# Kernel tuning notes

Measured on AMD Instinct MI355X. Metric: run time of the kernel, lower is better.

## Reference

```python
import jax, jax.numpy as jnp
import numpy as np
from jax import lax

B, T, C = 4, 1024, 1024
H, HEAD = 16, 64            # n_head, head size (K == V == HEAD)
TM_DIM, TD_DIM = 32, 64     # TIME_MIX_EXTRA_DIM, W_MIX_EXTRA_DIM
N_LAYER, LAYER_ID = 24, 12
EPS = 1e-5
HEAD_DIV = 8.0              # head_size_divisor


def setup_inputs() -> dict:
    key = jax.random.key(0)
    ks = jax.random.split(key, 10)
    r1 = 1.0 - LAYER_ID / N_LAYER          # ratio_1_to_almost0
    r0 = LAYER_ID / max(N_LAYER - 1, 1)    # ratio_0_to_1
    ddd = np.arange(C, dtype=np.float64) / C
    x_maa = (1.0 - ddd ** r1).astype(np.float32)
    r_maa = (1.0 - ddd ** (0.5 * r1)).astype(np.float32)
    v_maa = (1.0 - (ddd ** r1 + 0.3 * r0)).astype(np.float32)
    n = np.arange(H * HEAD, dtype=np.float64)
    denom = max(H * HEAD - 1, 1)
    time_decay = (-6.0 + 5.0 * (n / denom) ** (0.7 + 1.3 * r0)).reshape(H, HEAD).astype(np.float32)
    zig = (((np.arange(H * HEAD) + 1) % 3) - 1) * 0.1
    time_first = (r0 * (1.0 - n / denom) + zig).reshape(H, HEAD).astype(np.float32)

    def unif(k, shape, s=0.01):
        return jax.random.uniform(k, shape, jnp.float32, -s, s)

    return {
        "x": jax.random.normal(ks[0], (B, T, C), jnp.float32),
        "x_maa": jnp.asarray(x_maa),
        "w_maa": jnp.asarray(x_maa),
        "k_maa": jnp.asarray(x_maa),
        "v_maa": jnp.asarray(v_maa),
        "r_maa": jnp.asarray(r_maa),
        "g_maa": jnp.asarray(r_maa),
        "tm_w1": unif(ks[1], (C, 5 * TM_DIM)),
        "tm_w2": unif(ks[2], (5, TM_DIM, C)),
        "td_w1": unif(ks[3], (C, TD_DIM)),
        "td_w2": unif(ks[4], (TD_DIM, C)),
        "time_decay": jnp.asarray(time_decay),
        "time_first": jnp.asarray(time_first),
        "Wr": jax.random.normal(ks[5], (C, H * HEAD), jnp.float32) * 0.02,
        "Wk": jax.random.normal(ks[6], (C, H * HEAD), jnp.float32) * 0.02,
        "Wv": jax.random.normal(ks[7], (C, H * HEAD), jnp.float32) * 0.02,
        "Wg": jax.random.normal(ks[8], (C, H * HEAD), jnp.float32) * 0.02,
        "Wo": jax.random.normal(ks[9], (H * HEAD, C), jnp.float32) * 0.02,
        "ln_w": jnp.ones((H * HEAD,), jnp.float32),
        "ln_b": jnp.zeros((H * HEAD,), jnp.float32),
    }


def reference(x, x_maa, w_maa, k_maa, v_maa, r_maa, g_maa,
              tm_w1, tm_w2, td_w1, td_w2, time_decay, time_first,
              Wr, Wk, Wv, Wg, Wo, ln_w, ln_b):
    B, T, C = x.shape
    H, K = time_decay.shape
    V = Wv.shape[1] // H
    # token shift: sx = x_{t-1} - x_t (zero-padded at t=0)
    sx = jnp.concatenate([jnp.zeros_like(x[:, :1]), x[:, :-1]], axis=1) - x
    # data-dependent token-mix LoRA: 5 mixing deltas
    mix = jnp.tanh((x + sx * x_maa) @ tm_w1).reshape(B, T, 5, TM_DIM)
    mix = jnp.einsum('btfd,fdc->fbtc', mix, tm_w2)  # [5,B,T,C]
    mw, mk, mv, mr, mg = mix
    wx = x + sx * (w_maa + mw)
    kx = x + sx * (k_maa + mk)
    vx = x + sx * (v_maa + mv)
    rx = x + sx * (r_maa + mr)
    gx = x + sx * (g_maa + mg)
    r = (rx @ Wr).reshape(B, T, H, K)
    k = (kx @ Wk).reshape(B, T, H, K)
    v = (vx @ Wv).reshape(B, T, H, V)
    g = jax.nn.silu(gx @ Wg)                         # [B,T,H*V]
    # data-dependent decay via LoRA, then double-exp squash into (0,1)
    w = time_decay[None, None] + (jnp.tanh(wx @ td_w1) @ td_w2).reshape(B, T, H, K)
    w = jnp.exp(-jnp.exp(w))                         # [B,T,H,K]
    u = time_first                                   # [H,K]

    def step(s, inp):
        rt, kt, vt, wt = inp                         # [B,H,K],[B,H,K],[B,H,V],[B,H,K]
        kv = kt[..., None] * vt[..., None, :]        # [B,H,K,V] outer product
        y = jnp.einsum('bhk,bhkv->bhv', rt, s + u[None, :, :, None] * kv)
        return wt[..., None] * s + kv, y

    s0 = jnp.zeros((B, H, K, V), x.dtype)
    xs = (jnp.moveaxis(r, 1, 0), jnp.moveaxis(k, 1, 0),
          jnp.moveaxis(v, 1, 0), jnp.moveaxis(w, 1, 0))
    _, ys = lax.scan(step, s0, xs)                   # ys: [T,B,H,V]
    out = jnp.moveaxis(ys, 0, 1).reshape(B, T, H, V) / HEAD_DIV
    # GroupNorm with n_kv_head groups over dim_v channels -> per-head norm
    mu = out.mean(-1, keepdims=True)
    var = out.var(-1, keepdims=True)
    out = ((out - mu) * lax.rsqrt(var + EPS)).reshape(B, T, H * V) * ln_w + ln_b
    return (out * g) @ Wo
```

## Files before the change

### kernel.cpp

```cpp
#include <hip/hip_runtime.h>
#include <hip/hip_bf16.h>
#include <math.h>
#include <stdint.h>

constexpr int Bn = 4, Tn = 1024, Cn = 1024, Hn = 16;
constexpr int BT = Bn * Tn;
constexpr long long BTC = (long long)BT * Cn;
constexpr int CL = 64;
constexpr int NC = Tn / CL;

typedef __bf16 bf16x8_t __attribute__((ext_vector_type(8)));
typedef float f32x4_t __attribute__((ext_vector_type(4)));
typedef unsigned short us8_t __attribute__((ext_vector_type(8)));

__device__ __forceinline__ unsigned short f2bf_bits(float v) {
    __hip_bfloat16 h = __float2bfloat16(v);
    return *reinterpret_cast<unsigned short*>(&h);
}
__device__ __forceinline__ float bfbits2f(unsigned short u) {
    unsigned int x = (unsigned int)u << 16;
    return __uint_as_float(x);
}

__device__ __forceinline__ void gload16(const void* g, void* l) {
    auto const* gp = reinterpret_cast<const unsigned int __attribute__((address_space(1)))*>(
        reinterpret_cast<uintptr_t>(g));
    auto* lp = reinterpret_cast<unsigned int __attribute__((address_space(3)))*>(
        reinterpret_cast<uintptr_t>(l));
    __builtin_amdgcn_global_load_lds(gp, lp, 16, 0, 0);
}

__global__ __launch_bounds__(256) void prep_mixin(const float* __restrict__ x,
                                                  const float* __restrict__ x_maa,
                                                  __hip_bfloat16* __restrict__ out) {
    long long q = (long long)blockIdx.x * 256 + threadIdx.x;
    if (q * 4 >= BTC) return;
    long long idx = q * 4;
    int c = (int)(idx & (Cn - 1));
    long long bt = idx >> 10;
    int t = (int)(bt & (Tn - 1));
    float4 xv = *reinterpret_cast<const float4*>(x + idx);
    float4 xp = (t > 0) ? *reinterpret_cast<const float4*>(x + idx - Cn)
                        : make_float4(0.f, 0.f, 0.f, 0.f);
    float4 ma = *reinterpret_cast<const float4*>(x_maa + c);
    ushort4 o;
    o.x = f2bf_bits(xv.x + (xp.x - xv.x) * ma.x);
    o.y = f2bf_bits(xv.y + (xp.y - xv.y) * ma.y);
    o.z = f2bf_bits(xv.z + (xp.z - xv.z) * ma.z);
    o.w = f2bf_bits(xv.w + (xp.w - xv.w) * ma.w);
    *reinterpret_cast<ushort4*>(out + idx) = o;
}

__global__ __launch_bounds__(256) void transp5(const float* __restrict__ W0,
                                               const float* __restrict__ W1,
                                               const float* __restrict__ W2,
                                               const float* __restrict__ W3,
                                               const float* __restrict__ W4,
                                               __hip_bfloat16* __restrict__ T0,
                                               __hip_bfloat16* __restrict__ T1,
                                               __hip_bfloat16* __restrict__ T2,
                                               __hip_bfloat16* __restrict__ T3,
                                               __hip_bfloat16* __restrict__ T4) {
    int z = blockIdx.z;
    const float* W = (z == 0) ? W0 : (z == 1) ? W1 : (z == 2) ? W2 : (z == 3) ? W3 : W4;
    __hip_bfloat16* Wt = (z == 0) ? T0 : (z == 1) ? T1 : (z == 2) ? T2 : (z == 3) ? T3 : T4;
    __shared__ float tile[32][33];
    int c0 = blockIdx.x * 32, r0 = blockIdx.y * 32;
    int tx = threadIdx.x & 31, ty = threadIdx.x >> 5;
    #pragma unroll
    for (int i = 0; i < 4; i++)
        tile[ty + 8 * i][tx] = W[(size_t)(r0 + ty + 8 * i) * Cn + c0 + tx];
    __syncthreads();
    #pragma unroll
    for (int i = 0; i < 4; i++)
        Wt[(size_t)(c0 + ty + 8 * i) * Cn + r0 + tx] = __float2bfloat16(tile[tx][ty + 8 * i]);
}

__global__ __launch_bounds__(256) void transp_bf16(const float* __restrict__ W,
                                                   __hip_bfloat16* __restrict__ Wt,
                                                   int R, int Cc) {
    __shared__ float tile[32][33];
    int c0 = blockIdx.x * 32, r0 = blockIdx.y * 32;
    int tx = threadIdx.x & 31, ty = threadIdx.x >> 5;
    #pragma unroll
    for (int i = 0; i < 4; i++)
        tile[ty + 8 * i][tx] = W[(size_t)(r0 + ty + 8 * i) * Cc + c0 + tx];
    __syncthreads();
    #pragma unroll
    for (int i = 0; i < 4; i++)
        Wt[(size_t)(c0 + ty + 8 * i) * R + r0 + tx] = __float2bfloat16(tile[tx][ty + 8 * i]);
}

template <int EPI>
__global__ __launch_bounds__(256) void gemm_f32(const float* __restrict__ A,
                                                const float* __restrict__ Bm,
                                                float* __restrict__ C,
                                                int M, int N, int K,
                                                const float* __restrict__ extra) {
    __shared__ float As[16][64];
    __shared__ float Bs[16][64];
    int tid = threadIdx.x;
    int m0 = blockIdx.y * 64, n0 = blockIdx.x * 64;
    int tx = tid & 15, ty = tid >> 4;
    int ar = tid >> 2, ac = (tid & 3) * 4;
    int br = tid >> 4, bc = (tid & 15) * 4;
    float acc[4][4] = {};

    for (int k0 = 0; k0 < K; k0 += 16) {
        const float* ap = A + (size_t)(m0 + ar) * K + k0 + ac;
        float4 av = *reinterpret_cast<const float4*>(ap);
        As[ac + 0][ar] = av.x; As[ac + 1][ar] = av.y;
        As[ac + 2][ar] = av.z; As[ac + 3][ar] = av.w;
        float4 bv = *reinterpret_cast<const float4*>(Bm + (size_t)(k0 + br) * N + n0 + bc);
        *reinterpret_cast<float4*>(&Bs[br][bc]) = bv;
        __syncthreads();
        #pragma unroll
        for (int kk = 0; kk < 16; kk++) {
            float4 a4 = *reinterpret_cast<const float4*>(&As[kk][ty * 4]);
            float4 b4 = *reinterpret_cast<const float4*>(&Bs[kk][tx * 4]);
            float aa[4] = {a4.x, a4.y, a4.z, a4.w};
            float bb[4] = {b4.x, b4.y, b4.z, b4.w};
            #pragma unroll
            for (int i = 0; i < 4; i++)
                #pragma unroll
                for (int j = 0; j < 4; j++)
                    acc[i][j] = fmaf(aa[i], bb[j], acc[i][j]);
        }
        __syncthreads();
    }

    #pragma unroll
    for (int i = 0; i < 4; i++) {
        int row = m0 + ty * 4 + i;
        #pragma unroll
        for (int j = 0; j < 4; j++) {
            int col = n0 + tx * 4 + j;
            float v = acc[i][j];
            if (EPI == 3) v = -expf(extra[col] + v);
            C[(size_t)row * N + col] = v;
        }
    }
}

template <int KS>
__global__ __launch_bounds__(256) void gemm_f32_splitk(const float* __restrict__ A,
                                                       const float* __restrict__ Bm,
                                                       float* __restrict__ part,
                                                       int M, int N, int K) {
    __shared__ float As[16][64];
    __shared__ float Bs[16][64];
    int tid = threadIdx.x;
    int kp = blockIdx.x;
    int m0 = blockIdx.y * 64;
    int kbeg = kp * (K / KS), kend = kbeg + K / KS;
    int tx = tid & 15, ty = tid >> 4;
    int ar = tid >> 2, ac = (tid & 3) * 4;
    int br = tid >> 4, bc = (tid & 15) * 4;
    float acc[4][4] = {};

    for (int k0 = kbeg; k0 < kend; k0 += 16) {
        float4 av = *reinterpret_cast<const float4*>(A + (size_t)(m0 + ar) * K + k0 + ac);
        As[ac + 0][ar] = av.x; As[ac + 1][ar] = av.y;
        As[ac + 2][ar] = av.z; As[ac + 3][ar] = av.w;
        *reinterpret_cast<float4*>(&Bs[br][bc]) =
            *reinterpret_cast<const float4*>(Bm + (size_t)(k0 + br) * N + bc);
        __syncthreads();
        #pragma unroll
        for (int kk = 0; kk < 16; kk++) {
            float4 a4 = *reinterpret_cast<const float4*>(&As[kk][ty * 4]);
            float4 b4 = *reinterpret_cast<const float4*>(&Bs[kk][tx * 4]);
            float aa[4] = {a4.x, a4.y, a4.z, a4.w};
            float bb[4] = {b4.x, b4.y, b4.z, b4.w};
            #pragma unroll
            for (int i = 0; i < 4; i++)
                #pragma unroll
                for (int j = 0; j < 4; j++)
                    acc[i][j] = fmaf(aa[i], bb[j], acc[i][j]);
        }
        __syncthreads();
    }
    #pragma unroll
    for (int i = 0; i < 4; i++) {
        int row = m0 + ty * 4 + i;
        #pragma unroll
        for (int j = 0; j < 4; j++)
            part[((size_t)kp * M + row) * N + tx * 4 + j] = acc[i][j];
    }
}

template <int KS>
__global__ __launch_bounds__(256) void splitk_reduce_tanh(const float* __restrict__ part,
                                                          float* __restrict__ outp,
                                                          int total, size_t stride) {
    int i = blockIdx.x * 256 + threadIdx.x;
    if (i >= total) return;
    float s = 0.f;
    #pragma unroll
    for (int kp = 0; kp < KS; kp++) s += part[kp * stride + i];
    outp[i] = tanhf(s);
}

template <int KS>
__global__ __launch_bounds__(256) void splitk_reduce_tanh_bf(const float* __restrict__ part,
                                                             __hip_bfloat16* __restrict__ outp,
                                                             int total, size_t stride) {
    int i = blockIdx.x * 256 + threadIdx.x;
    if (i >= total) return;
    float s = 0.f;
    #pragma unroll
    for (int kp = 0; kp < KS; kp++) s += part[kp * stride + i];
    outp[i] = __float2bfloat16(tanhf(s));
}

template <int KS>
__global__ __launch_bounds__(256) void gemm_mfma_sk(const __hip_bfloat16* __restrict__ A,
                                                    const __hip_bfloat16* __restrict__ Bt,
                                                    float* __restrict__ part,
                                                    int M, int N, int K) {
    __shared__ alignas(16) unsigned short As[64 * 64];
    __shared__ alignas(16) unsigned short Bs[128 * 64];
    int tid = threadIdx.x;
    int m0 = blockIdx.y * 64, n0 = blockIdx.x * 128;
    int kp = blockIdx.z;
    int kbeg = kp * (K / KS), kend = kbeg + K / KS;
    int wave = tid >> 6, lane = tid & 63;
    int wm = (wave & 1) * 32, wn = (wave >> 1) * 64;
    int l15 = lane & 15, l4 = lane >> 4;
    f32x4_t acc[2][4] = {};

    for (int k0 = kbeg; k0 < kend; k0 += 64) {
        #pragma unroll
        for (int p = 0; p < 2; p++) {
            int cch = tid + p * 256;
            int row = cch >> 3, slot = cch & 7;
            int s2 = slot ^ (row & 7);
            *reinterpret_cast<us8_t*>(&As[row * 64 + s2 * 8]) =
                *reinterpret_cast<const us8_t*>(&A[(size_t)(m0 + row) * K + k0 + slot * 8]);
        }
        #pragma unroll
        for (int p = 0; p < 4; p++) {
            int cch = tid + p * 256;
            int row = cch >> 3, slot = cch & 7;
            int s2 = slot ^ (row & 7);
            int rowg = n0 + row; if (rowg > N - 1) rowg = N - 1;
            *reinterpret_cast<us8_t*>(&Bs[row * 64 + s2 * 8]) =
                *reinterpret_cast<const us8_t*>(&Bt[(size_t)rowg * K + k0 + slot * 8]);
        }
        __syncthreads();
        #pragma unroll
        for (int kw = 0; kw < 2; kw++) {
            int slot = kw * 4 + l4;
            bf16x8_t af[2], bfr[4];
            #pragma unroll
            for (int f = 0; f < 2; f++) {
                int ar = wm + f * 16 + l15;
                af[f] = *reinterpret_cast<const bf16x8_t*>(&As[ar * 64 + (slot ^ (ar & 7)) * 8]);
            }
            #pragma unroll
            for (int f = 0; f < 4; f++) {
                int br = wn + f * 16 + l15;
                bfr[f] = *reinterpret_cast<const bf16x8_t*>(&Bs[br * 64 + (slot ^ (br & 7)) * 8]);
            }
            #pragma unroll
            for (int i = 0; i < 2; i++)
                #pragma unroll
                for (int j = 0; j < 4; j++)
                    acc[i][j] = __builtin_amdgcn_mfma_f32_16x16x32_bf16(af[i], bfr[j], acc[i][j], 0, 0, 0);
        }
        __syncthreads();
    }

    #pragma unroll
    for (int i = 0; i < 2; i++) {
        int rbase = m0 + wm + i * 16 + l4 * 4;
        #pragma unroll
        for (int j = 0; j < 4; j++) {
            int col = n0 + wn + j * 16 + l15;
            if (col < N) {
                #pragma unroll
                for (int q = 0; q < 4; q++)
                    part[((size_t)kp * M + rbase + q) * N + col] = acc[i][j][q];
            }
        }
    }
}

__global__ __launch_bounds__(256) void dmix_gemm(const __hip_bfloat16* __restrict__ A,
                                                 const __hip_bfloat16* __restrict__ W2T,
                                                 __hip_bfloat16* __restrict__ D) {
    __shared__ alignas(16) unsigned short As[64 * 32];
    __shared__ alignas(16) unsigned short Bs[128 * 32];
    int tid = threadIdx.x;
    int m0 = blockIdx.x * 64, n0 = blockIdx.y * 128;
    int f  = blockIdx.z;
    int wave = tid >> 6, lane = tid & 63;
    int wm = (wave & 1) * 32, wn = (wave >> 1) * 64;
    int l15 = lane & 15, l4 = lane >> 4;
    int lrow2 = lane >> 2, ls = lane & 3;
    f32x4_t acc[2][4] = {};

    {
        int row = wave * 16 + lrow2;
        int gs = ls ^ (row & 3);
        gload16(&A[(size_t)(m0 + row) * 160 + f * 32 + gs * 8], &As[(wave * 16) * 32]);
    }
    #pragma unroll
    for (int ci = 0; ci < 2; ci++) {
        int r0 = wave * 32 + ci * 16;
        int row = r0 + lrow2;
        int gs = ls ^ (row & 3);
        gload16(&W2T[(size_t)(n0 + row) * 160 + f * 32 + gs * 8], &Bs[r0 * 32]);
    }
    __syncthreads();
    bf16x8_t af[2], bfr[4];
    #pragma unroll
    for (int i = 0; i < 2; i++) {
        int ar = wm + i * 16 + l15;
        af[i] = *reinterpret_cast<const bf16x8_t*>(&As[ar * 32 + ((l4 ^ (ar & 3)) * 8)]);
    }
    #pragma unroll
    for (int j = 0; j < 4; j++) {
        int br = wn + j * 16 + l15;
        bfr[j] = *reinterpret_cast<const bf16x8_t*>(&Bs[br * 32 + ((l4 ^ (br & 3)) * 8)]);
    }
    #pragma unroll
    for (int i = 0; i < 2; i++)
        #pragma unroll
        for (int j = 0; j < 4; j++)
            acc[i][j] = __builtin_amdgcn_mfma_f32_16x16x32_bf16(af[i], bfr[j], acc[i][j], 0, 0, 0);

    __hip_bfloat16* Df = D + (size_t)f * BTC;
    #pragma unroll
    for (int i = 0; i < 2; i++) {
        int rbase = m0 + wm + i * 16 + l4 * 4;
        #pragma unroll
        for (int j = 0; j < 4; j++) {
            int col = n0 + wn + j * 16 + l15;
            #pragma unroll
            for (int q = 0; q < 4; q++)
                Df[(size_t)(rbase + q) * Cn + col] = __float2bfloat16(acc[i][j][q]);
        }
    }
}

__global__ __launch_bounds__(256) void dmix_fuse(const float* __restrict__ x,
                                                 const __hip_bfloat16* __restrict__ D,
                                                 const float* __restrict__ wmaa,
                                                 const float* __restrict__ kmaa,
                                                 const float* __restrict__ vmaa,
                                                 const float* __restrict__ rmaa,
                                                 const float* __restrict__ gmaa,
                                                 float* __restrict__ wx,
                                                 __hip_bfloat16* __restrict__ kxb,
                                                 __hip_bfloat16* __restrict__ vxb,
                                                 __hip_bfloat16* __restrict__ rxb,
                                                 __hip_bfloat16* __restrict__ gxb) {
    long long q = (long long)blockIdx.x * 256 + threadIdx.x;
    if (q * 4 >= BTC) return;
    long long idx = q * 4;
    int c = (int)(idx & (Cn - 1));
    int t = (int)((idx >> 10) & (Tn - 1));
    float4 xv = *reinterpret_cast<const float4*>(x + idx);
    float4 xp = (t > 0) ? *reinterpret_cast<const float4*>(x + idx - Cn)
                        : make_float4(0.f, 0.f, 0.f, 0.f);
    float sx[4] = {xp.x - xv.x, xp.y - xv.y, xp.z - xv.z, xp.w - xv.w};
    float xvv[4] = {xv.x, xv.y, xv.z, xv.w};
    #pragma unroll
    for (int f = 0; f < 5; f++) {
        const float* maa = (f == 0) ? wmaa : (f == 1) ? kmaa : (f == 2) ? vmaa
                         : (f == 3) ? rmaa : gmaa;
        float4 m4 = *reinterpret_cast<const float4*>(maa + c);
        float mm[4] = {m4.x, m4.y, m4.z, m4.w};
        ushort4 d4 = *reinterpret_cast<const ushort4*>(D + (size_t)f * BTC + idx);
        float dd[4] = {bfbits2f(d4.x), bfbits2f(d4.y), bfbits2f(d4.z), bfbits2f(d4.w)};
        float val[4];
        #pragma unroll
        for (int j = 0; j < 4; j++) val[j] = xvv[j] + sx[j] * (mm[j] + dd[j]);
        if (f == 0) {
            *reinterpret_cast<float4*>(wx + idx) = make_float4(val[0], val[1], val[2], val[3]);
        } else {
            ushort4 o;
            o.x = f2bf_bits(val[0]); o.y = f2bf_bits(val[1]);
            o.z = f2bf_bits(val[2]); o.w = f2bf_bits(val[3]);
            __hip_bfloat16* dst = (f == 1) ? kxb : (f == 2) ? vxb : (f == 3) ? rxb : gxb;
            *reinterpret_cast<ushort4*>(dst + idx) = o;
        }
    }
}

__global__ __launch_bounds__(256) void gemm_qkvg(const __hip_bfloat16* __restrict__ A0,
                                                 const __hip_bfloat16* __restrict__ A1,
                                                 const __hip_bfloat16* __restrict__ A2,
                                                 const __hip_bfloat16* __restrict__ A3,
                                                 const __hip_bfloat16* __restrict__ B0,
                                                 const __hip_bfloat16* __restrict__ B1,
                                                 const __hip_bfloat16* __restrict__ B2,
                                                 const __hip_bfloat16* __restrict__ B3,
                                                 __hip_bfloat16* __restrict__ C0,
                                                 __hip_bfloat16* __restrict__ C1,
                                                 __hip_bfloat16* __restrict__ C2,
                                                 __hip_bfloat16* __restrict__ C3,
                                                 int M, int N, int K) {
    int g = blockIdx.z;
    const __hip_bfloat16* A  = (g == 0) ? A0 : (g == 1) ? A1 : (g == 2) ? A2 : A3;
    const __hip_bfloat16* Bt = (g == 0) ? B0 : (g == 1) ? B1 : (g == 2) ? B2 : B3;
    __hip_bfloat16* Co = (g == 0) ? C0 : (g == 1) ? C1 : (g == 2) ? C2 : C3;
    __shared__ alignas(16) unsigned short As[64 * 64];
    __shared__ alignas(16) unsigned short Bs[128 * 64];
    int tid = threadIdx.x;
    int m0 = blockIdx.x * 64, n0 = blockIdx.y * 128;
    int wave = tid >> 6, lane = tid & 63;
    int wm = (wave & 1) * 32, wn = (wave >> 1) * 64;
    int l15 = lane & 15, l4 = lane >> 4;
    int lrow = lane >> 3, ls2 = lane & 7;
    f32x4_t acc[2][4] = {};

    for (int k0 = 0; k0 < K; k0 += 64) {
        #pragma unroll
        for (int ci = 0; ci < 2; ci++) {
            int r0 = wave * 16 + ci * 8;
            int row = r0 + lrow;
            int gs = ls2 ^ (row & 7);
            gload16(&A[(size_t)(m0 + row) * K + k0 + gs * 8], &As[r0 * 64]);
        }
        #pragma unroll
        for (int ci = 0; ci < 4; ci++) {
            int r0 = wave * 32 + ci * 8;
            int row = r0 + lrow;
            int gs = ls2 ^ (row & 7);
            gload16(&Bt[(size_t)(n0 + row) * K + k0 + gs * 8], &Bs[r0 * 64]);
        }
        __syncthreads();
        #pragma unroll
        for (int kw = 0; kw < 2; kw++) {
            int slot = kw * 4 + l4;
            bf16x8_t af[2], bfr[4];
            #pragma unroll
            for (int f = 0; f < 2; f++) {
                int ar = wm + f * 16 + l15;
                af[f] = *reinterpret_cast<const bf16x8_t*>(&As[ar * 64 + (slot ^ (ar & 7)) * 8]);
            }
            #pragma unroll
            for (int f = 0; f < 4; f++) {
                int br = wn + f * 16 + l15;
                bfr[f] = *reinterpret_cast<const bf16x8_t*>(&Bs[br * 64 + (slot ^ (br & 7)) * 8]);
            }
            #pragma unroll
            for (int i = 0; i < 2; i++)
                #pragma unroll
                for (int j = 0; j < 4; j++)
                    acc[i][j] = __builtin_amdgcn_mfma_f32_16x16x32_bf16(af[i], bfr[j], acc[i][j], 0, 0, 0);
        }
        __syncthreads();
    }

    #pragma unroll
    for (int i = 0; i < 2; i++) {
        int rbase = m0 + wm + i * 16 + l4 * 4;
        #pragma unroll
        for (int j = 0; j < 4; j++) {
            int col = n0 + wn + j * 16 + l15;
            #pragma unroll
            for (int q = 0; q < 4; q++) {
                float v = acc[i][j][q];
                if (g == 3) v = v / (1.f + expf(-v));
                Co[(size_t)(rbase + q) * N + col] = __float2bfloat16(v);
            }
        }
    }
}

__global__ __launch_bounds__(256) void gemm_mfma_gl(const __hip_bfloat16* __restrict__ A,
                                                    const __hip_bfloat16* __restrict__ Bt,
                                                    float* __restrict__ Cout,
                                                    int M, int N, int K) {
    __shared__ alignas(16) unsigned short As[64 * 64];
    __shared__ alignas(16) unsigned short Bs[128 * 64];
    int tid = threadIdx.x;
    int m0 = blockIdx.x * 64, n0 = blockIdx.y * 128;
    int wave = tid >> 6, lane = tid & 63;
    int wm = (wave & 1) * 32, wn = (wave >> 1) * 64;
    int l15 = lane & 15, l4 = lane >> 4;
    int lrow = lane >> 3, ls2 = lane & 7;
    f32x4_t acc[2][4] = {};

    for (int k0 = 0; k0 < K; k0 += 64) {
        #pragma unroll
        for (int ci = 0; ci < 2; ci++) {
            int r0 = wave * 16 + ci * 8;
            int row = r0 + lrow;
            int gs = ls2 ^ (row & 7);
            gload16(&A[(size_t)(m0 + row) * K + k0 + gs * 8], &As[r0 * 64]);
        }
        #pragma unroll
        for (int ci = 0; ci < 4; ci++) {
            int r0 = wave * 32 + ci * 8;
            int row = r0 + lrow;
            int gs = ls2 ^ (row & 7);
            gload16(&Bt[(size_t)(n0 + row) * K + k0 + gs * 8], &Bs[r0 * 64]);
        }
        __syncthreads();
        #pragma unroll
        for (int kw = 0; kw < 2; kw++) {
            int slot = kw * 4 + l4;
            bf16x8_t af[2], bfr[4];
            #pragma unroll
            for (int f = 0; f < 2; f++) {
                int ar = wm + f * 16 + l15;
                af[f] = *reinterpret_cast<const bf16x8_t*>(&As[ar * 64 + (slot ^ (ar & 7)) * 8]);
            }
            #pragma unroll
            for (int f = 0; f < 4; f++) {
                int br = wn + f * 16 + l15;
                bfr[f] = *reinterpret_cast<const bf16x8_t*>(&Bs[br * 64 + (slot ^ (br & 7)) * 8]);
            }
            #pragma unroll
            for (int i = 0; i < 2; i++)
                #pragma unroll
                for (int j = 0; j < 4; j++)
                    acc[i][j] = __builtin_amdgcn_mfma_f32_16x16x32_bf16(af[i], bfr[j], acc[i][j], 0, 0, 0);
        }
        __syncthreads();
    }

    #pragma unroll
    for (int i = 0; i < 2; i++) {
        int rbase = m0 + wm + i * 16 + l4 * 4;
        #pragma unroll
        for (int j = 0; j < 4; j++) {
            int col = n0 + wn + j * 16 + l15;
            #pragma unroll
            for (int q = 0; q < 4; q++)
                Cout[(size_t)(rbase + q) * N + col] = acc[i][j][q];
        }
    }
}

__global__ __launch_bounds__(256) void chunk_summary(const __hip_bfloat16* __restrict__ kb,
                                                     const __hip_bfloat16* __restrict__ vb,
                                                     const float* __restrict__ lw,
                                                     float* __restrict__ Bc,
                                                     float* __restrict__ Wtot) {
    int bid = blockIdx.x;
    int c = bid & 15, h = (bid >> 4) & 15, b = bid >> 8;
    size_t gbase = ((size_t)(b * Tn + c * CL) * Hn + h) * 64;
    int tid = threadIdx.x;
    __shared__ float linc[64][68];
    __shared__ float wtp[4][64];
    __shared__ alignas(16) __hip_bfloat16 kdT[64][72];
    __shared__ alignas(16) __hip_bfloat16 vsT[64][72];
    int wave = tid >> 6, lane = tid & 63;
    {
        float acc = 0.f;
        #pragma unroll
        for (int i = 0; i < 16; i++) {
            int t = wave * 16 + i;
            acc += lw[gbase + (size_t)t * 1024 + lane];
            linc[t][lane] = acc;
        }
        wtp[wave][lane] = acc;
    }
    __syncthreads();
    {
        float off = 0.f;
        for (int g = 0; g < wave; g++) off += wtp[g][lane];
        #pragma unroll
        for (int i = 0; i < 16; i++) linc[wave * 16 + i][lane] += off;
    }
    __syncthreads();
    int t4 = tid >> 2, c0 = (tid & 3) * 16;
    #pragma unroll
    for (int i = 0; i < 4; i++) {
        int ch = c0 + i * 4;
        size_t ga = gbase + (size_t)t4 * 1024 + ch;
        ushort4 ku = *reinterpret_cast<const ushort4*>(kb + ga);
        ushort4 vu = *reinterpret_cast<const ushort4*>(vb + ga);
        float kk[4] = {bfbits2f(ku.x), bfbits2f(ku.y), bfbits2f(ku.z), bfbits2f(ku.w)};
        float vv[4] = {bfbits2f(vu.x), bfbits2f(vu.y), bfbits2f(vu.z), bfbits2f(vu.w)};
        #pragma unroll
        for (int j = 0; j < 4; j++) {
            float li = linc[t4][ch + j];
            float lend = linc[63][ch + j];
            kdT[ch + j][t4] = __float2bfloat16(kk[j] * expf(lend - li));
            vsT[ch + j][t4] = __float2bfloat16(vv[j]);
        }
    }
    if (tid < 64) Wtot[(size_t)bid * 64 + tid] = expf(linc[63][tid]);
    __syncthreads();
    int l15 = lane & 15, l4q = lane >> 4;
    #pragma unroll
    for (int nt = 0; nt < 4; nt++) {
        f32x4_t acc = {};
        #pragma unroll
        for (int kt = 0; kt < 2; kt++) {
            bf16x8_t a = *reinterpret_cast<const bf16x8_t*>(&kdT[wave * 16 + l15][kt * 32 + l4q * 8]);
            bf16x8_t bb = *reinterpret_cast<const bf16x8_t*>(&vsT[nt * 16 + l15][kt * 32 + l4q * 8]);
            acc = __builtin_amdgcn_mfma_f32_16x16x32_bf16(a, bb, acc, 0, 0, 0);
        }
        #pragma unroll
        for (int q = 0; q < 4; q++) {
            int krow = wave * 16 + l4q * 4 + q;
            Bc[(size_t)bid * 4096 + (size_t)krow * 64 + nt * 16 + l15] = acc[q];
        }
    }
}

__global__ __launch_bounds__(256) void chunk_scan(const float* __restrict__ Bc,
                                                  const float* __restrict__ Wtot,
                                                  float* __restrict__ SbufT) {
    int bid = blockIdx.x;
    int bh = bid >> 2, vg = bid & 3;
    int kk = threadIdx.x >> 2;
    int v = vg * 16 + (threadIdx.x & 3) * 4;
    float4 S = make_float4(0.f, 0.f, 0.f, 0.f);
    for (int c = 0; c < NC; c++) {
        size_t base = (size_t)(bh * NC + c) * 4096;
        SbufT[base + (size_t)(v + 0) * 64 + kk] = S.x;
        SbufT[base + (size_t)(v + 1) * 64 + kk] = S.y;
        SbufT[base + (size_t)(v + 2) * 64 + kk] = S.z;
        SbufT[base + (size_t)(v + 3) * 64 + kk] = S.w;
        float wt = Wtot[(size_t)(bh * NC + c) * 64 + kk];
        float4 b4 = *reinterpret_cast<const float4*>(Bc + base + (size_t)kk * 64 + v);
        S.x = fmaf(wt, S.x, b4.x);
        S.y = fmaf(wt, S.y, b4.y);
        S.z = fmaf(wt, S.z, b4.z);
        S.w = fmaf(wt, S.w, b4.w);
    }
}

__global__ __launch_bounds__(256) void chunk_out(const __hip_bfloat16* __restrict__ rb,
                                                 const __hip_bfloat16* __restrict__ kb,
                                                 const __hip_bfloat16* __restrict__ vb,
                                                 const float* __restrict__ lw,
                                                 const float* __restrict__ SbufT,
                                                 const float* __restrict__ tf,
                                                 float* __restrict__ y) {
    int bid = blockIdx.x;
    int c = bid & 15, h = (bid >> 4) & 15, b = bid >> 8;
    size_t gbase = ((size_t)(b * Tn + c * CL) * Hn + h) * 64;
    int tid = threadIdx.x;
    __shared__ alignas(16) __hip_bfloat16 qs[64][72];
    __shared__ alignas(16) __hip_bfloat16 ks[64][72];
    __shared__ alignas(16) __hip_bfloat16 vsT[64][72];
    __shared__ alignas(16) __hip_bfloat16 scT[64][72];
    __shared__ alignas(16) float uni[64 * 68];
    __shared__ float wtp[4][64];
    __shared__ float diag[64];
    float (*linc)[68] = reinterpret_cast<float(*)[68]>(uni);
    __hip_bfloat16 (*asb)[72] = reinterpret_cast<__hip_bfloat16(*)[72]>(uni);
    int wave = tid >> 6, lane = tid & 63;
    {
        float acc = 0.f;
        #pragma unroll
        for (int i = 0; i < 16; i++) {
            int t = wave * 16 + i;
            acc += lw[gbase + (size_t)t * 1024 + lane];
            linc[t][lane] = acc;
        }
        wtp[wave][lane] = acc;
    }
    __syncthreads();
    {
        float off = 0.f;
        for (int g = 0; g < wave; g++) off += wtp[g][lane];
        #pragma unroll
        for (int i = 0; i < 16; i++) linc[wave * 16 + i][lane] += off;
    }
    __syncthreads();
    int t4 = tid >> 2, c0 = (tid & 3) * 16;
    float dpart = 0.f;
    #pragma unroll
    for (int i = 0; i < 4; i++) {
        int ch = c0 + i * 4;
        size_t ga = gbase + (size_t)t4 * 1024 + ch;
        ushort4 ru = *reinterpret_cast<const ushort4*>(rb + ga);
        ushort4 ku = *reinterpret_cast<const ushort4*>(kb + ga);
        ushort4 vu = *reinterpret_cast<const ushort4*>(vb + ga);
        float4 l4v = *reinterpret_cast<const float4*>(lw + ga);
        float4 u4 = *reinterpret_cast<const float4*>(tf + h * 64 + ch);
        float4 s4 = *reinterpret_cast<const float4*>(SbufT + (size_t)bid * 4096 + (size_t)t4 * 64 + ch);
        float rr[4] = {bfbits2f(ru.x), bfbits2f(ru.y), bfbits2f(ru.z), bfbits2f(ru.w)};
        float kkv[4] = {bfbits2f(ku.x), bfbits2f(ku.y), bfbits2f(ku.z), bfbits2f(ku.w)};
        float vv[4] = {bfbits2f(vu.x), bfbits2f(vu.y), bfbits2f(vu.z), bfbits2f(vu.w)};
        float lwv[4] = {l4v.x, l4v.y, l4v.z, l4v.w};
        float uu[4] = {u4.x, u4.y, u4.z, u4.w};
        float ss[4] = {s4.x, s4.y, s4.z, s4.w};
        #pragma unroll
        for (int j = 0; j < 4; j++) {
            float li = linc[t4][ch + j];
            qs[t4][ch + j] = __float2bfloat16(rr[j] * expf(li - lwv[j]));
            ks[t4][ch + j] = __float2bfloat16(kkv[j] * expf(-li));
            vsT[ch + j][t4] = __float2bfloat16(vv[j]);
            scT[t4][ch + j] = __float2bfloat16(ss[j]);
            dpart = fmaf(rr[j] * uu[j], kkv[j], dpart);
        }
    }
    dpart += __shfl_xor(dpart, 1);
    dpart += __shfl_xor(dpart, 2);
    if ((tid & 3) == 0) diag[t4] = dpart;
    __syncthreads();
    int l15 = lane & 15, l4q = lane >> 4;
    #pragma unroll
    for (int nt = 0; nt < 4; nt++) {
        f32x4_t acc = {};
        if (nt <= wave) {
            #pragma unroll
            for (int kt = 0; kt < 2; kt++) {
                bf16x8_t a = *reinterpret_cast<const bf16x8_t*>(&qs[wave * 16 + l15][kt * 32 + l4q * 8]);
                bf16x8_t bb = *reinterpret_cast<const bf16x8_t*>(&ks[nt * 16 + l15][kt * 32 + l4q * 8]);
                acc = __builtin_amdgcn_mfma_f32_16x16x32_bf16(a, bb, acc, 0, 0, 0);
            }
        }
        #pragma unroll
        for (int q = 0; q < 4; q++) {
            int t = wave * 16 + l4q * 4 + q;
            int tau = nt * 16 + l15;
            float v = (tau < t) ? acc[q] : (tau == t ? diag[t] : 0.f);
            asb[t][tau] = __float2bfloat16(v);
        }
    }
    __syncthreads();
    #pragma unroll
    for (int nt = 0; nt < 4; nt++) {
        f32x4_t acc = {};
        int kmax = (wave >> 1) + 1;
        for (int kt = 0; kt < kmax; kt++) {
            bf16x8_t a = *reinterpret_cast<const bf16x8_t*>(&asb[wave * 16 + l15][kt * 32 + l4q * 8]);
            bf16x8_t bb = *reinterpret_cast<const bf16x8_t*>(&vsT[nt * 16 + l15][kt * 32 + l4q * 8]);
            acc = __builtin_amdgcn_mfma_f32_16x16x32_bf16(a, bb, acc, 0, 0, 0);
        }
        #pragma unroll
        for (int kt = 0; kt < 2; kt++) {
            bf16x8_t a = *reinterpret_cast<const bf16x8_t*>(&qs[wave * 16 + l15][kt * 32 + l4q * 8]);
            bf16x8_t bb = *reinterpret_cast<const bf16x8_t*>(&scT[nt * 16 + l15][kt * 32 + l4q * 8]);
            acc = __builtin_amdgcn_mfma_f32_16x16x32_bf16(a, bb, acc, 0, 0, 0);
        }
        #pragma unroll
        for (int q = 0; q < 4; q++) {
            int t = wave * 16 + l4q * 4 + q;
            y[gbase + (size_t)t * 1024 + nt * 16 + l15] = acc[q];
        }
    }
}

__global__ __launch_bounds__(256) void gn_mul(const float* __restrict__ y,
                                              const __hip_bfloat16* __restrict__ g,
                                              const float* __restrict__ lnw,
                                              const float* __restrict__ lnb,
                                              __hip_bfloat16* __restrict__ fin) {
    int tid = threadIdx.x;
    int lane = tid & 63;
    int wv = tid >> 6;
    int grp = blockIdx.x * 4 + wv;
    int h = grp & 15;
    size_t idx = (size_t)grp * 64 + lane;
    float val = y[idx] * 0.125f;
    float sum = val, sq = val * val;
    #pragma unroll
    for (int off = 32; off > 0; off >>= 1) {
        sum += __shfl_xor(sum, off, 64);
        sq  += __shfl_xor(sq,  off, 64);
    }
    float mu = sum * (1.f / 64.f);
    float var = sq * (1.f / 64.f) - mu * mu;
    float rs = rsqrtf(var + 1e-5f);
    float o = (val - mu) * rs * lnw[h * 64 + lane] + lnb[h * 64 + lane];
    fin[idx] = __float2bfloat16(o * __bfloat162float(g[idx]));
}

extern "C" void kernel_launch(void* const* d_in, const int* in_sizes, int n_in,
                              void* d_out, int out_size, void* d_ws, size_t ws_size,
                              hipStream_t stream) {
    (void)in_sizes; (void)n_in; (void)out_size; (void)ws_size;
    const float* x      = (const float*)d_in[0];
    const float* x_maa  = (const float*)d_in[1];
    const float* w_maa  = (const float*)d_in[2];
    const float* k_maa  = (const float*)d_in[3];
    const float* v_maa  = (const float*)d_in[4];
    const float* r_maa  = (const float*)d_in[5];
    const float* g_maa  = (const float*)d_in[6];
    const float* tm_w1  = (const float*)d_in[7];
    const float* tm_w2  = (const float*)d_in[8];
    const float* td_w1  = (const float*)d_in[9];
    const float* td_w2  = (const float*)d_in[10];
    const float* t_dec  = (const float*)d_in[11];
    const float* t_first= (const float*)d_in[12];
    const float* Wr     = (const float*)d_in[13];
    const float* Wk     = (const float*)d_in[14];
    const float* Wv     = (const float*)d_in[15];
    const float* Wg     = (const float*)d_in[16];
    const float* Wo     = (const float*)d_in[17];
    const float* ln_w   = (const float*)d_in[18];
    const float* ln_b   = (const float*)d_in[19];
    float* out = (float*)d_out;

    char* ws = (char*)d_ws;
    size_t off = 0;
    auto alloc = [&](size_t bytes) -> void* {
        void* p = ws + off;
        off = (off + bytes + 255) & ~(size_t)255;
        return p;
    };
    __hip_bfloat16* mixin = (__hip_bfloat16*)alloc(BTC * 2);
    __hip_bfloat16* mix160b = (__hip_bfloat16*)alloc((size_t)BT * 160 * 2);
    float* wxr    = (float*)alloc(BTC * 4);
    __hip_bfloat16* kxb = (__hip_bfloat16*)alloc(BTC * 2);
    __hip_bfloat16* vxb = (__hip_bfloat16*)alloc(BTC * 2);
    __hip_bfloat16* rxb = (__hip_bfloat16*)alloc(BTC * 2);
    __hip_bfloat16* gxb = (__hip_bfloat16*)alloc(BTC * 2);
    __hip_bfloat16* kb  = (__hip_bfloat16*)alloc(BTC * 2);
    __hip_bfloat16* vb  = (__hip_bfloat16*)alloc(BTC * 2);
    __hip_bfloat16* gb  = (__hip_bfloat16*)alloc(BTC * 2);
    float* wl1 = (float*)alloc((size_t)BT * 64 * 4);
    float* lwb = (float*)alloc(BTC * 4);
    __hip_bfloat16* WrT = (__hip_bfloat16*)alloc((size_t)Cn * Cn * 2);
    __hip_bfloat16* WkT = (__hip_bfloat16*)alloc((size_t)Cn * Cn * 2);
    __hip_bfloat16* WvT = (__hip_bfloat16*)alloc((size_t)Cn * Cn * 2);
    __hip_bfloat16* WgT = (__hip_bfloat16*)alloc((size_t)Cn * Cn * 2);
    __hip_bfloat16* WoT = (__hip_bfloat16*)alloc((size_t)Cn * Cn * 2);
    __hip_bfloat16* tmw1T = (__hip_bfloat16*)alloc((size_t)160 * Cn * 2);
    __hip_bfloat16* w2T   = (__hip_bfloat16*)alloc((size_t)Cn * 160 * 2);
    char* big = (char*)alloc((size_t)5 * BTC * 2);
    float* lorapart = (float*)big;
    __hip_bfloat16* d5 = (__hip_bfloat16*)big;
    float* skpart = (float*)big;
    __hip_bfloat16* rb = mixin;
    float* BcB   = wxr;
    float* ybuf  = wxr;
    float* WtB   = wl1;
    float* SbufT = (float*)rxb;
    __hip_bfloat16* fin = kxb;

    dim3 blk(256);
    transp5<<<dim3(32, 32, 5), blk, 0, stream>>>(Wr, Wk, Wv, Wg, Wo,
                                                 WrT, WkT, WvT, WgT, WoT);
    transp_bf16<<<dim3(5, 32), blk, 0, stream>>>(tm_w1, tmw1T, Cn, 160);
    transp_bf16<<<dim3(32, 5), blk, 0, stream>>>(tm_w2, w2T, 160, Cn);
    prep_mixin<<<dim3((unsigned)(BTC / 1024)), blk, 0, stream>>>(x, x_maa, mixin);
    gemm_mfma_sk<4><<<dim3(2, 64, 4), blk, 0, stream>>>(mixin, tmw1T, lorapart, BT, 160, Cn);
    splitk_reduce_tanh_bf<4><<<dim3((BT * 160 + 255) / 256), blk, 0, stream>>>(
        lorapart, mix160b, BT * 160, (size_t)BT * 160);
    dmix_gemm<<<dim3(64, 8, 5), blk, 0, stream>>>(mix160b, w2T, d5);
    dmix_fuse<<<dim3((unsigned)(BTC / 1024)), blk, 0, stream>>>(x, d5,
                                                                w_maa, k_maa, v_maa, r_maa, g_maa,
                                                                wxr, kxb, vxb, rxb, gxb);
    gemm_qkvg<<<dim3(64, 8, 4), blk, 0, stream>>>(rxb, kxb, vxb, gxb,
                                                  WrT, WkT, WvT, WgT,
                                                  rb, kb, vb, gb, BT, Cn, Cn);
    gemm_f32_splitk<8><<<dim3(8, 64), blk, 0, stream>>>(wxr, td_w1, skpart, BT, 64, Cn);
    splitk_reduce_tanh<8><<<dim3(BT * 64 / 256), blk, 0, stream>>>(skpart, wl1, BT * 64,
                                                                   (size_t)BT * 64);
    gemm_f32<3><<<dim3(16, 64), blk, 0, stream>>>(wl1, td_w2, lwb, BT, Cn, 64, t_dec);
    chunk_summary<<<dim3(Bn * Hn * NC), blk, 0, stream>>>(kb, vb, lwb, BcB, WtB);
    chunk_scan<<<dim3(Bn * Hn * 4), blk, 0, stream>>>(BcB, WtB, SbufT);
    chunk_out<<<dim3(Bn * Hn * NC), blk, 0, stream>>>(rb, kb, vb, lwb, SbufT, t_first, ybuf);
    gn_mul<<<dim3(BT * Hn / 4), blk, 0, stream>>>(ybuf, gb, ln_w, ln_b, fin);
    gemm_mfma_gl<<<dim3(64, 8), blk, 0, stream>>>(fin, WoT, out, BT, Cn, Cn);
}
```

Measured before the change: 211.6 us.

## Fuse GroupNorm-gate into chunk_out and merge decay LoRA split-K into QKVG launch

The per-head GroupNorm, ln affine and gate multiply now run inside chunk_out. Each wave reduces row statistics across its 16 lanes with shuffles and writes the bf16 result directly, so the fp32 y buffer round trip and the separate gn_mul kernel go away. The fp32 split-K GEMM for the decay LoRA first stage now runs as an extra z-slice (g==4) of the gemm_qkvg grid, reusing its shared memory. This removes a launch and lets that small GEMM overlap with the QKVG tiles, at the cost of branch divergence across blocks and possible load imbalance inside the merged grid.

```diff
diff --git a/kernel.cpp b/kernel.cpp
--- a/kernel.cpp
+++ b/kernel.cpp
@@ -139,52 +139,6 @@
             if (EPI == 3) v = -expf(extra[col] + v);
             C[(size_t)row * N + col] = v;
         }
-    }
-}
-
-template <int KS>
-__global__ __launch_bounds__(256) void gemm_f32_splitk(const float* __restrict__ A,
-                                                       const float* __restrict__ Bm,
-                                                       float* __restrict__ part,
-                                                       int M, int N, int K) {
-    __shared__ float As[16][64];
-    __shared__ float Bs[16][64];
-    int tid = threadIdx.x;
-    int kp = blockIdx.x;
-    int m0 = blockIdx.y * 64;
-    int kbeg = kp * (K / KS), kend = kbeg + K / KS;
-    int tx = tid & 15, ty = tid >> 4;
-    int ar = tid >> 2, ac = (tid & 3) * 4;
-    int br = tid >> 4, bc = (tid & 15) * 4;
-    float acc[4][4] = {};
-
-    for (int k0 = kbeg; k0 < kend; k0 += 16) {
-        float4 av = *reinterpret_cast<const float4*>(A + (size_t)(m0 + ar) * K + k0 + ac);
-        As[ac + 0][ar] = av.x; As[ac + 1][ar] = av.y;
-        As[ac + 2][ar] = av.z; As[ac + 3][ar] = av.w;
-        *reinterpret_cast<float4*>(&Bs[br][bc]) =
-            *reinterpret_cast<const float4*>(Bm + (size_t)(k0 + br) * N + bc);
-        __syncthreads();
-        #pragma unroll
-        for (int kk = 0; kk < 16; kk++) {
-            float4 a4 = *reinterpret_cast<const float4*>(&As[kk][ty * 4]);
-            float4 b4 = *reinterpret_cast<const float4*>(&Bs[kk][tx * 4]);
-            float aa[4] = {a4.x, a4.y, a4.z, a4.w};
-            float bb[4] = {b4.x, b4.y, b4.z, b4.w};
-            #pragma unroll
-            for (int i = 0; i < 4; i++)
-                #pragma unroll
-                for (int j = 0; j < 4; j++)
-                    acc[i][j] = fmaf(aa[i], bb[j], acc[i][j]);
-        }
-        __syncthreads();
-    }
-    #pragma unroll
-    for (int i = 0; i < 4; i++) {
-        int row = m0 + ty * 4 + i;
-        #pragma unroll
-        for (int j = 0; j < 4; j++)
-            part[((size_t)kp * M + row) * N + tx * 4 + j] = acc[i][j];
     }
 }
 
@@ -400,14 +354,59 @@
                                                  __hip_bfloat16* __restrict__ C1,
                                                  __hip_bfloat16* __restrict__ C2,
                                                  __hip_bfloat16* __restrict__ C3,
-                                                 int M, int N, int K) {
+                                                 int M, int N, int K,
+                                                 const float* __restrict__ Af32,
+                                                 const float* __restrict__ Btd,
+                                                 float* __restrict__ part) {
+    __shared__ alignas(16) unsigned short As[64 * 64];
+    __shared__ alignas(16) unsigned short Bs[128 * 64];
     int g = blockIdx.z;
+    int tid = threadIdx.x;
+
+    if (g == 4) {
+        float (*Asf)[64] = reinterpret_cast<float(*)[64]>(As);
+        float (*Bsf)[64] = reinterpret_cast<float(*)[64]>(Bs);
+        int kp = blockIdx.y;
+        int m0 = blockIdx.x * 64;
+        int kbeg = kp * 128, kend = kbeg + 128;
+        int tx = tid & 15, ty = tid >> 4;
+        int ar = tid >> 2, ac = (tid & 3) * 4;
+        int br = tid >> 4, bc = (tid & 15) * 4;
+        float facc[4][4] = {};
+        for (int k0 = kbeg; k0 < kend; k0 += 16) {
+            float4 av = *reinterpret_cast<const float4*>(Af32 + (size_t)(m0 + ar) * 1024 + k0 + ac);
+            Asf[ac + 0][ar] = av.x; Asf[ac + 1][ar] = av.y;
+            Asf[ac + 2][ar] = av.z; Asf[ac + 3][ar] = av.w;
+            *reinterpret_cast<float4*>(&Bsf[br][bc]) =
+                *reinterpret_cast<const float4*>(Btd + (size_t)(k0 + br) * 64 + bc);
+            __syncthreads();
+            #pragma unroll
+            for (int kk = 0; kk < 16; kk++) {
+                float4 a4 = *reinterpret_cast<const float4*>(&Asf[kk][ty * 4]);
+                float4 b4 = *reinterpret_cast<const float4*>(&Bsf[kk][tx * 4]);
+                float aa[4] = {a4.x, a4.y, a4.z, a4.w};
+                float bb[4] = {b4.x, b4.y, b4.z, b4.w};
+                #pragma unroll
+                for (int i = 0; i < 4; i++)
+                    #pragma unroll
+                    for (int j = 0; j < 4; j++)
+                        facc[i][j] = fmaf(aa[i], bb[j], facc[i][j]);
+            }
+            __syncthreads();
+        }
+        #pragma unroll
+        for (int i = 0; i < 4; i++) {
+            int row = m0 + ty * 4 + i;
+            #pragma unroll
+            for (int j = 0; j < 4; j++)
+                part[((size_t)kp * BT + row) * 64 + tx * 4 + j] = facc[i][j];
+        }
+        return;
+    }
+
     const __hip_bfloat16* A  = (g == 0) ? A0 : (g == 1) ? A1 : (g == 2) ? A2 : A3;
     const __hip_bfloat16* Bt = (g == 0) ? B0 : (g == 1) ? B1 : (g == 2) ? B2 : B3;
     __hip_bfloat16* Co = (g == 0) ? C0 : (g == 1) ? C1 : (g == 2) ? C2 : C3;
-    __shared__ alignas(16) unsigned short As[64 * 64];
-    __shared__ alignas(16) unsigned short Bs[128 * 64];
-    int tid = threadIdx.x;
     int m0 = blockIdx.x * 64, n0 = blockIdx.y * 128;
     int wave = tid >> 6, lane = tid & 63;
     int wm = (wave & 1) * 32, wn = (wave >> 1) * 64;
@@ -634,7 +633,10 @@
                                                  const float* __restrict__ lw,
                                                  const float* __restrict__ SbufT,
                                                  const float* __restrict__ tf,
-                                                 float* __restrict__ y) {
+                                                 const __hip_bfloat16* __restrict__ gb,
+                                                 const float* __restrict__ lnw,
+                                                 const float* __restrict__ lnb,
+                                                 __hip_bfloat16* __restrict__ fin) {
     int bid = blockIdx.x;
     int c = bid & 15, h = (bid >> 4) & 15, b = bid >> 8;
     size_t gbase = ((size_t)(b * Tn + c * CL) * Hn + h) * 64;
@@ -720,6 +722,7 @@
         }
     }
     __syncthreads();
+    f32x4_t oacc[4];
     #pragma unroll
     for (int nt = 0; nt < 4; nt++) {
         f32x4_t acc = {};
@@ -735,37 +738,46 @@
             bf16x8_t bb = *reinterpret_cast<const bf16x8_t*>(&scT[nt * 16 + l15][kt * 32 + l4q * 8]);
             acc = __builtin_amdgcn_mfma_f32_16x16x32_bf16(a, bb, acc, 0, 0, 0);
         }
+        oacc[nt] = acc;
+    }
+    float sum[4] = {0.f, 0.f, 0.f, 0.f}, sq[4] = {0.f, 0.f, 0.f, 0.f};
+    #pragma unroll
+    for (int nt = 0; nt < 4; nt++)
+        #pragma unroll
+        for (int q = 0; q < 4; q++) {
+            float v = oacc[nt][q] * 0.125f;
+            oacc[nt][q] = v;
+            sum[q] += v;
+            sq[q] += v * v;
+        }
+    #pragma unroll
+    for (int off = 1; off < 16; off <<= 1)
+        #pragma unroll
+        for (int q = 0; q < 4; q++) {
+            sum[q] += __shfl_xor(sum[q], off, 64);
+            sq[q]  += __shfl_xor(sq[q],  off, 64);
+        }
+    float mu[4], rs[4];
+    #pragma unroll
+    for (int q = 0; q < 4; q++) {
+        mu[q] = sum[q] * (1.f / 64.f);
+        float var = sq[q] * (1.f / 64.f) - mu[q] * mu[q];
+        rs[q] = rsqrtf(var + 1e-5f);
+    }
+    #pragma unroll
+    for (int nt = 0; nt < 4; nt++) {
+        int v = nt * 16 + l15;
+        float lw_ = lnw[h * 64 + v];
+        float lb_ = lnb[h * 64 + v];
         #pragma unroll
         for (int q = 0; q < 4; q++) {
             int t = wave * 16 + l4q * 4 + q;
-            y[gbase + (size_t)t * 1024 + nt * 16 + l15] = acc[q];
-        }
-    }
-}
-
-__global__ __launch_bounds__(256) void gn_mul(const float* __restrict__ y,
-                                              const __hip_bfloat16* __restrict__ g,
-                                              const float* __restrict__ lnw,
-                                              const float* __restrict__ lnb,
-                                              __hip_bfloat16* __restrict__ fin) {
-    int tid = threadIdx.x;
-    int lane = tid & 63;
-    int wv = tid >> 6;
-    int grp = blockIdx.x * 4 + wv;
-    int h = grp & 15;
-    size_t idx = (size_t)grp * 64 + lane;
-    float val = y[idx] * 0.125f;
-    float sum = val, sq = val * val;
-    #pragma unroll
-    for (int off = 32; off > 0; off >>= 1) {
-        sum += __shfl_xor(sum, off, 64);
-        sq  += __shfl_xor(sq,  off, 64);
-    }
-    float mu = sum * (1.f / 64.f);
-    float var = sq * (1.f / 64.f) - mu * mu;
-    float rs = rsqrtf(var + 1e-5f);
-    float o = (val - mu) * rs * lnw[h * 64 + lane] + lnb[h * 64 + lane];
-    fin[idx] = __float2bfloat16(o * __bfloat162float(g[idx]));
+            size_t o = gbase + (size_t)t * 1024 + v;
+            float gv = bfbits2f(*reinterpret_cast<const unsigned short*>(&gb[o]));
+            float val = (oacc[nt][q] - mu[q]) * rs[q] * lw_ + lb_;
+            fin[o] = __float2bfloat16(val * gv);
+        }
+    }
 }
 
 extern "C" void kernel_launch(void* const* d_in, const int* in_sizes, int n_in,
@@ -826,7 +838,6 @@
     float* skpart = (float*)big;
     __hip_bfloat16* rb = mixin;
     float* BcB   = wxr;
-    float* ybuf  = wxr;
     float* WtB   = wl1;
     float* SbufT = (float*)rxb;
     __hip_bfloat16* fin = kxb;
@@ -844,16 +855,16 @@
     dmix_fuse<<<dim3((unsigned)(BTC / 1024)), blk, 0, stream>>>(x, d5,
                                                                 w_maa, k_maa, v_maa, r_maa, g_maa,
                                                                 wxr, kxb, vxb, rxb, gxb);
-    gemm_qkvg<<<dim3(64, 8, 4), blk, 0, stream>>>(rxb, kxb, vxb, gxb,
+    gemm_qkvg<<<dim3(64, 8, 5), blk, 0, stream>>>(rxb, kxb, vxb, gxb,
                                                   WrT, WkT, WvT, WgT,
-                                                  rb, kb, vb, gb, BT, Cn, Cn);
-    gemm_f32_splitk<8><<<dim3(8, 64), blk, 0, stream>>>(wxr, td_w1, skpart, BT, 64, Cn);
+                                                  rb, kb, vb, gb, BT, Cn, Cn,
+                                                  wxr, td_w1, skpart);
     splitk_reduce_tanh<8><<<dim3(BT * 64 / 256), blk, 0, stream>>>(skpart, wl1, BT * 64,
                                                                    (size_t)BT * 64);
     gemm_f32<3><<<dim3(16, 64), blk, 0, stream>>>(wl1, td_w2, lwb, BT, Cn, 64, t_dec);
     chunk_summary<<<dim3(Bn * Hn * NC), blk, 0, stream>>>(kb, vb, lwb, BcB, WtB);
     chunk_scan<<<dim3(Bn * Hn * 4), blk, 0, stream>>>(BcB, WtB, SbufT);
-    chunk_out<<<dim3(Bn * Hn * NC), blk, 0, stream>>>(rb, kb, vb, lwb, SbufT, t_first, ybuf);
-    gn_mul<<<dim3(BT * Hn / 4), blk, 0, stream>>>(ybuf, gb, ln_w, ln_b, fin);
+    chunk_out<<<dim3(Bn * Hn * NC), blk, 0, stream>>>(rb, kb, vb, lwb, SbufT, t_first,
+                                                      gb, ln_w, ln_b, fin);
     gemm_mfma_gl<<<dim3(64, 8), blk, 0, stream>>>(fin, WoT, out, BT, Cn, Cn);
 }
```

After: 215.6 us. Within noise of the previous version (+1.9%).
